# Kernel optimization log

Hardware: AMD Instinct MI355X
Metric: run time of the kernel (lower is better)

Reference implementation:

```python
import jax, jax.numpy as jnp
import numpy as np

N_BINS = 11
Q_LEN = 50
EMB = 50      # == dim_term_gating
BATCH = 256
D_LEN = 2000
EPS = 1e-8


def setup_inputs() -> dict:
    key = jax.random.key(0)
    ks = jax.random.split(key, 6)
    q_embeddings = jax.random.normal(ks[0], (BATCH, Q_LEN, EMB), jnp.float32)
    d_embeddings = jax.random.normal(ks[1], (BATCH, D_LEN, EMB), jnp.float32)
    q_embeddings_ids = jax.random.randint(ks[2], (BATCH, Q_LEN), 0, 30000)
    d_embeddings_ids = jax.random.randint(ks[3], (BATCH, D_LEN), 0, 30000)
    # linear1: Linear(n_bins*q_len, 1); gating: Linear(emb*q_len, 1, bias=False)
    W1 = jax.random.normal(ks[4], (N_BINS * Q_LEN,), jnp.float32) * 0.02
    b1 = jnp.zeros((1,), jnp.float32)
    Wg = jax.random.normal(ks[5], (EMB * Q_LEN,), jnp.float32) * 0.02
    return {
        "q_embeddings": q_embeddings,
        "d_embeddings": d_embeddings,
        "W1": W1,
        "b1": b1,
        "Wg": Wg,
        "q_embeddings_ids": q_embeddings_ids,
        "d_embeddings_ids": d_embeddings_ids,
    }


def reference(q_embeddings, d_embeddings, W1, b1, Wg, q_embeddings_ids, d_embeddings_ids):
    B, Q, E = q_embeddings.shape
    D = d_embeddings.shape[1]

    # ---- DrmmSimmat: cosine similarity between every query/doc term ----
    qn = q_embeddings / (jnp.linalg.norm(q_embeddings, axis=-1, keepdims=True) + EPS)
    dn = d_embeddings / (jnp.linalg.norm(d_embeddings, axis=-1, keepdims=True) + EPS)
    sim = jnp.einsum("bqe,bde->bqd", qn, dn)  # [B, Q, D]

    # ---- DrmmHistogram: per-query-term log-count histogram over [-1,1] ----
    # valid positions: token id != 0 (padding) in both query and doc dims
    valid = ((q_embeddings_ids > 0)[:, :, None] & (d_embeddings_ids > 0)[:, None, :])
    valid = valid.astype(jnp.float32)  # [B, Q, D]
    bins = jnp.clip(((sim + 1.000001) * 0.5 * (N_BINS - 1)).astype(jnp.int32), 0, N_BINS - 1)
    row = jnp.arange(B * Q, dtype=jnp.int32).reshape(B, Q, 1)  # histogram row per (b, q)
    flat_idx = (row * N_BINS + bins).reshape(-1)
    hist = jnp.zeros((B * Q * N_BINS,), jnp.float32).at[flat_idx].add(valid.reshape(-1))
    hist = jnp.log(hist + 1e-5).reshape(B, Q * N_BINS)

    # ---- feed-forward + term gating ----
    out_ffn = hist @ W1 + b1[0]                      # [B]
    gate = q_embeddings.reshape(B, Q * E) @ Wg       # [B]
    out_tgn = jax.nn.softmax(gate)                   # softmax over batch (faithful to F.softmax on squeezed [B])
    # torch broadcast (B,1)*(B,) -> (B,B); sum over dim=1
    matching_score = jnp.sum(out_ffn[:, None] * out_tgn[None, :], axis=1)  # [B]
    return matching_score
```

## Files before the change

### kernel.cpp

```cpp
#include <hip/hip_runtime.h>
#include <math.h>

#define BATCH 256
#define QL 50
#define EMB 50
#define DL 2000
#define NB 11
#define SEG 16
#define RPB 125
#define TPB 256
#define NKP 25
#define HB (QL * NB)

#define FOR_M5(M) M(0) M(1) M(2) M(3) M(4)
#define FOR_MN(M) \
  M(0,0) M(0,1) M(0,2) M(0,3) M(0,4) \
  M(1,0) M(1,1) M(1,2) M(1,3) M(1,4) \
  M(2,0) M(2,1) M(2,2) M(2,3) M(2,4) \
  M(3,0) M(3,1) M(3,2) M(3,3) M(3,4) \
  M(4,0) M(4,1) M(4,2) M(4,3) M(4,4)

#define DECL_ACC(m,n) float a_##m##_##n = 0.f;
#define LOAD_Q(m) const float2 qv##m = s_q2[kq + qg5 + m];
#define LOAD_D(n) const float2 dv##n = s_d2[kd + rg5 + n];
#define FMA2(m,n) a_##m##_##n = fmaf(qv##m.x, dv##n.x, a_##m##_##n); \
                  a_##m##_##n = fmaf(qv##m.y, dv##n.y, a_##m##_##n);
#define HIST_MN(m,n) if (qv_##m && dv_##n) { \
    const float s_  = a_##m##_##n * qrn##m * drn##n; \
    const float tt_ = ((s_ + 1.000001f) * 0.5f) * 10.0f; \
    int bb_ = (int)tt_; bb_ = bb_ < 0 ? 0 : (bb_ > 10 ? 10 : bb_); \
    atomicAdd(&s_hist[(qg5 + m) * NB + bb_], 1u); }

__global__ __launch_bounds__(TPB)
void sim_hist_kernel(const float* __restrict__ de,
                     const int*   __restrict__ did,
                     const float* __restrict__ qe,
                     const int*   __restrict__ qid,
                     const float* __restrict__ Wg,
                     unsigned char* __restrict__ g_hist,
                     float* __restrict__ gate,
                     int* __restrict__ cnt)
{
    const int bid = blockIdx.x;
    const int b   = bid >> 4;
    const int seg = bid & 15;
    const int t   = threadIdx.x;

    __shared__ float2   s_d2[NKP * RPB];
    __shared__ float2   s_q2[NKP * QL];
    __shared__ float    s_qrn[QL];
    __shared__ float    s_drn[RPB];
    __shared__ int      s_qv[QL];
    __shared__ int      s_dval[RPB];
    __shared__ unsigned s_hist[HB];
    __shared__ float    r2s[4];

    if (bid == 0 && t == 0) *cnt = 0;
    for (int i = t; i < HB; i += TPB) s_hist[i] = 0u;

    const float* dbase = de + ((size_t)b * DL + seg * RPB) * EMB;
    for (int i = t; i < NKP * RPB; i += TPB) {
        const int r  = i / NKP;
        const int ep = i - r * NKP;
        s_d2[ep * RPB + r] = *(const float2*)(dbase + r * EMB + 2 * ep);
    }
    const float* qbase = qe + (size_t)b * QL * EMB;
    for (int i = t; i < NKP * QL; i += TPB) {
        const int q  = i / NKP;
        const int ep = i - q * NKP;
        s_q2[ep * QL + q] = *(const float2*)(qbase + q * EMB + 2 * ep);
    }
    __syncthreads();

    if (t < RPB) {
        float ss = 0.f;
        #pragma unroll
        for (int ep = 0; ep < NKP; ++ep) {
            const float2 v = s_d2[ep * RPB + t];
            ss = fmaf(v.x, v.x, ss);
            ss = fmaf(v.y, v.y, ss);
        }
        s_drn[t]  = 1.0f / (sqrtf(ss) + 1e-8f);
        s_dval[t] = (did[(size_t)b * DL + seg * RPB + t] > 0) ? 1 : 0;
    }
    if (t < QL) {
        float ss = 0.f;
        #pragma unroll
        for (int ep = 0; ep < NKP; ++ep) {
            const float2 v = s_q2[ep * QL + t];
            ss = fmaf(v.x, v.x, ss);
            ss = fmaf(v.y, v.y, ss);
        }
        s_qrn[t] = 1.0f / (sqrtf(ss) + 1e-8f);
        s_qv[t]  = (qid[(size_t)b * QL + t] > 0) ? 1 : 0;
    }
    __syncthreads();

    if (t < 250) {
        const int qg5 = (t % 10) * 5;
        const int rg5 = (t / 10) * 5;
        FOR_MN(DECL_ACC)
        #pragma unroll 1
        for (int kp = 0; kp < NKP; ++kp) {
            const int kq = kp * QL;
            const int kd = kp * RPB;
            FOR_M5(LOAD_Q)
            FOR_M5(LOAD_D)
            FOR_MN(FMA2)
        }
        const float qrn0 = s_qrn[qg5+0], qrn1 = s_qrn[qg5+1], qrn2 = s_qrn[qg5+2],
                    qrn3 = s_qrn[qg5+3], qrn4 = s_qrn[qg5+4];
        const float drn0 = s_drn[rg5+0], drn1 = s_drn[rg5+1], drn2 = s_drn[rg5+2],
                    drn3 = s_drn[rg5+3], drn4 = s_drn[rg5+4];
        const int qv_0 = s_qv[qg5+0], qv_1 = s_qv[qg5+1], qv_2 = s_qv[qg5+2],
                  qv_3 = s_qv[qg5+3], qv_4 = s_qv[qg5+4];
        const int dv_0 = s_dval[rg5+0], dv_1 = s_dval[rg5+1], dv_2 = s_dval[rg5+2],
                  dv_3 = s_dval[rg5+3], dv_4 = s_dval[rg5+4];
        FOR_MN(HIST_MN)
    }
    __syncthreads();

    unsigned char* hout = g_hist + ((size_t)b * SEG + seg) * HB;
    for (int i = t; i < HB; i += TPB) hout[i] = (unsigned char)s_hist[i];

    if (seg == 0) {
        float a2 = 0.f;
        for (int i = t; i < QL * EMB; i += TPB)
            a2 = fmaf(qbase[i], Wg[i], a2);
        #pragma unroll
        for (int off = 32; off > 0; off >>= 1) a2 += __shfl_down(a2, off, 64);
        if ((t & 63) == 0) r2s[t >> 6] = a2;
        __syncthreads();
        if (t == 0) gate[b] = r2s[0] + r2s[1] + r2s[2] + r2s[3];
    }
}

__global__ __launch_bounds__(TPB)
void ffn_score_kernel(const unsigned char* __restrict__ g_hist,
                      const float* __restrict__ W1,
                      const float* __restrict__ bias,
                      const float* __restrict__ gate,
                      float* __restrict__ ffn,
                      int* __restrict__ cnt,
                      float* __restrict__ out)
{
    const int b = blockIdx.x;
    const int t = threadIdx.x;
    const unsigned char* hb = g_hist + (size_t)b * SEG * HB;

    float a1 = 0.f;
    for (int i = t; i < HB; i += TPB) {
        unsigned c = 0;
        #pragma unroll
        for (int s = 0; s < SEG; ++s) c += hb[s * HB + i];
        a1 = fmaf(logf((float)c + 1e-5f), W1[i], a1);
    }
    #pragma unroll
    for (int off = 32; off > 0; off >>= 1) a1 += __shfl_down(a1, off, 64);
    __shared__ float r1s[4];
    __shared__ int   s_last;
    if ((t & 63) == 0) r1s[t >> 6] = a1;
    __syncthreads();
    if (t == 0) {
        const float v = r1s[0] + r1s[1] + r1s[2] + r1s[3] + bias[0];
        atomicExch(&ffn[b], v);
        __threadfence();
        const int old = atomicAdd(cnt, 1);
        s_last = (old == BATCH - 1) ? 1 : 0;
    }
    __syncthreads();
    if (!s_last) return;
    __threadfence();

    __shared__ float buf[4];
    __shared__ float sM, sZ, sS;
    const float g = gate[t];
    const float f = atomicAdd(&ffn[t], 0.0f);

    float m = g;
    #pragma unroll
    for (int off = 32; off > 0; off >>= 1) m = fmaxf(m, __shfl_down(m, off, 64));
    if ((t & 63) == 0) buf[t >> 6] = m;
    __syncthreads();
    if (t == 0) sM = fmaxf(fmaxf(buf[0], buf[1]), fmaxf(buf[2], buf[3]));
    __syncthreads();

    const float e = expf(g - sM);
    float z = e;
    #pragma unroll
    for (int off = 32; off > 0; off >>= 1) z += __shfl_down(z, off, 64);
    __syncthreads();
    if ((t & 63) == 0) buf[t >> 6] = z;
    __syncthreads();
    if (t == 0) sZ = buf[0] + buf[1] + buf[2] + buf[3];
    __syncthreads();

    const float p = e / sZ;
    float s = p;
    #pragma unroll
    for (int off = 32; off > 0; off >>= 1) s += __shfl_down(s, off, 64);
    __syncthreads();
    if ((t & 63) == 0) buf[t >> 6] = s;
    __syncthreads();
    if (t == 0) sS = buf[0] + buf[1] + buf[2] + buf[3];
    __syncthreads();

    out[t] = f * sS;
}

extern "C" void kernel_launch(void* const* d_in, const int* in_sizes, int n_in,
                              void* d_out, int out_size, void* d_ws, size_t ws_size,
                              hipStream_t stream)
{
    const float* qe  = (const float*)d_in[0];
    const float* de  = (const float*)d_in[1];
    const float* W1  = (const float*)d_in[2];
    const float* b1  = (const float*)d_in[3];
    const float* Wg  = (const float*)d_in[4];
    const int*   qid = (const int*)d_in[5];
    const int*   did = (const int*)d_in[6];
    float* out = (float*)d_out;

    char* ws = (char*)d_ws;
    unsigned char* g_hist = (unsigned char*)ws;
    float* gate = (float*)(ws + 2252800);
    float* ffn  = gate + BATCH;
    int*   cnt  = (int*)(ffn + BATCH);

    sim_hist_kernel<<<BATCH * SEG, TPB, 0, stream>>>(de, did, qe, qid, Wg,
                                                     g_hist, gate, cnt);
    ffn_score_kernel<<<BATCH, TPB, 0, stream>>>(g_hist, W1, b1, gate, ffn, cnt, out);
}
```

Before: 234.3 us.

## Store tiles row-major with padded stride, use float4 LDS reads, fuse norm into load

Shared-memory tiles for doc and query embeddings move from a k-major float2 layout to a row-major layout with a padded stride of 52. This allows float4 LDS reads in the 5x5 register-tiled dot product, so the inner loop runs 12 iterations plus a tail instead of 25. The global-to-shared copy is now done per row by the same threads that compute the inverse norms, which removes one barrier but makes the global reads uncoalesced (one thread per row). Launch bounds now request 4 blocks per CU and the validity flags shrink to bytes.

Result: faster. 194.0 us (-17.2%).

```diff
diff --git a/kernel.cpp b/kernel.cpp
--- a/kernel.cpp
+++ b/kernel.cpp
@@ -9,7 +9,7 @@
 #define SEG 16
 #define RPB 125
 #define TPB 256
-#define NKP 25
+#define RSTRIDE 52
 #define HB (QL * NB)
 
 #define FOR_M5(M) M(0) M(1) M(2) M(3) M(4)
@@ -21,17 +21,25 @@
   M(4,0) M(4,1) M(4,2) M(4,3) M(4,4)
 
 #define DECL_ACC(m,n) float a_##m##_##n = 0.f;
-#define LOAD_Q(m) const float2 qv##m = s_q2[kq + qg5 + m];
-#define LOAD_D(n) const float2 dv##n = s_d2[kd + rg5 + n];
-#define FMA2(m,n) a_##m##_##n = fmaf(qv##m.x, dv##n.x, a_##m##_##n); \
-                  a_##m##_##n = fmaf(qv##m.y, dv##n.y, a_##m##_##n);
+#define LOAD_Q4(m) const float4 qv##m = *(const float4*)(qb0 + (m) * RSTRIDE + 4 * k);
+#define LOAD_D4(n) const float4 dv##n = *(const float4*)(db0 + (n) * RSTRIDE + 4 * k);
+#define LOAD_Q2(m) const float2 qt##m = *(const float2*)(qb0 + (m) * RSTRIDE + 48);
+#define LOAD_D2(n) const float2 dt##n = *(const float2*)(db0 + (n) * RSTRIDE + 48);
+#define FMA4(m,n) \
+  a_##m##_##n = fmaf(qv##m.x, dv##n.x, a_##m##_##n); \
+  a_##m##_##n = fmaf(qv##m.y, dv##n.y, a_##m##_##n); \
+  a_##m##_##n = fmaf(qv##m.z, dv##n.z, a_##m##_##n); \
+  a_##m##_##n = fmaf(qv##m.w, dv##n.w, a_##m##_##n);
+#define FMA2T(m,n) \
+  a_##m##_##n = fmaf(qt##m.x, dt##n.x, a_##m##_##n); \
+  a_##m##_##n = fmaf(qt##m.y, dt##n.y, a_##m##_##n);
 #define HIST_MN(m,n) if (qv_##m && dv_##n) { \
     const float s_  = a_##m##_##n * qrn##m * drn##n; \
     const float tt_ = ((s_ + 1.000001f) * 0.5f) * 10.0f; \
     int bb_ = (int)tt_; bb_ = bb_ < 0 ? 0 : (bb_ > 10 ? 10 : bb_); \
     atomicAdd(&s_hist[(qg5 + m) * NB + bb_], 1u); }
 
-__global__ __launch_bounds__(TPB)
+__global__ __launch_bounds__(TPB, 4)
 void sim_hist_kernel(const float* __restrict__ de,
                      const int*   __restrict__ did,
                      const float* __restrict__ qe,
@@ -46,67 +54,64 @@
     const int seg = bid & 15;
     const int t   = threadIdx.x;
 
-    __shared__ float2   s_d2[NKP * RPB];
-    __shared__ float2   s_q2[NKP * QL];
-    __shared__ float    s_qrn[QL];
-    __shared__ float    s_drn[RPB];
-    __shared__ int      s_qv[QL];
-    __shared__ int      s_dval[RPB];
-    __shared__ unsigned s_hist[HB];
-    __shared__ float    r2s[4];
+    __shared__ __align__(16) float s_d[RPB * RSTRIDE];
+    __shared__ __align__(16) float s_q[QL * RSTRIDE];
+    __shared__ float         s_drn[RPB];
+    __shared__ float         s_qrn[QL];
+    __shared__ unsigned char s_dval[RPB];
+    __shared__ unsigned char s_qv[QL];
+    __shared__ unsigned      s_hist[HB];
+    __shared__ float         r2s[4];
 
     if (bid == 0 && t == 0) *cnt = 0;
     for (int i = t; i < HB; i += TPB) s_hist[i] = 0u;
 
-    const float* dbase = de + ((size_t)b * DL + seg * RPB) * EMB;
-    for (int i = t; i < NKP * RPB; i += TPB) {
-        const int r  = i / NKP;
-        const int ep = i - r * NKP;
-        s_d2[ep * RPB + r] = *(const float2*)(dbase + r * EMB + 2 * ep);
-    }
-    const float* qbase = qe + (size_t)b * QL * EMB;
-    for (int i = t; i < NKP * QL; i += TPB) {
-        const int q  = i / NKP;
-        const int ep = i - q * NKP;
-        s_q2[ep * QL + q] = *(const float2*)(qbase + q * EMB + 2 * ep);
-    }
-    __syncthreads();
-
     if (t < RPB) {
+        const float* src = de + ((size_t)b * DL + seg * RPB + t) * EMB;
+        float* dst = s_d + t * RSTRIDE;
         float ss = 0.f;
         #pragma unroll
-        for (int ep = 0; ep < NKP; ++ep) {
-            const float2 v = s_d2[ep * RPB + t];
+        for (int ep = 0; ep < 25; ++ep) {
+            const float2 v = *(const float2*)(src + 2 * ep);
             ss = fmaf(v.x, v.x, ss);
             ss = fmaf(v.y, v.y, ss);
+            *(float2*)(dst + 2 * ep) = v;
         }
         s_drn[t]  = 1.0f / (sqrtf(ss) + 1e-8f);
         s_dval[t] = (did[(size_t)b * DL + seg * RPB + t] > 0) ? 1 : 0;
-    }
-    if (t < QL) {
+    } else if (t >= 128 && t < 128 + QL) {
+        const int j = t - 128;
+        const float* src = qe + ((size_t)b * QL + j) * EMB;
+        float* dst = s_q + j * RSTRIDE;
         float ss = 0.f;
         #pragma unroll
-        for (int ep = 0; ep < NKP; ++ep) {
-            const float2 v = s_q2[ep * QL + t];
+        for (int ep = 0; ep < 25; ++ep) {
+            const float2 v = *(const float2*)(src + 2 * ep);
             ss = fmaf(v.x, v.x, ss);
             ss = fmaf(v.y, v.y, ss);
-        }
-        s_qrn[t] = 1.0f / (sqrtf(ss) + 1e-8f);
-        s_qv[t]  = (qid[(size_t)b * QL + t] > 0) ? 1 : 0;
+            *(float2*)(dst + 2 * ep) = v;
+        }
+        s_qrn[j] = 1.0f / (sqrtf(ss) + 1e-8f);
+        s_qv[j]  = (qid[(size_t)b * QL + j] > 0) ? 1 : 0;
     }
     __syncthreads();
 
     if (t < 250) {
         const int qg5 = (t % 10) * 5;
         const int rg5 = (t / 10) * 5;
+        const float* qb0 = s_q + qg5 * RSTRIDE;
+        const float* db0 = s_d + rg5 * RSTRIDE;
         FOR_MN(DECL_ACC)
         #pragma unroll 1
-        for (int kp = 0; kp < NKP; ++kp) {
-            const int kq = kp * QL;
-            const int kd = kp * RPB;
-            FOR_M5(LOAD_Q)
-            FOR_M5(LOAD_D)
-            FOR_MN(FMA2)
+        for (int k = 0; k < 12; ++k) {
+            FOR_M5(LOAD_Q4)
+            FOR_M5(LOAD_D4)
+            FOR_MN(FMA4)
+        }
+        {
+            FOR_M5(LOAD_Q2)
+            FOR_M5(LOAD_D2)
+            FOR_MN(FMA2T)
         }
         const float qrn0 = s_qrn[qg5+0], qrn1 = s_qrn[qg5+1], qrn2 = s_qrn[qg5+2],
                     qrn3 = s_qrn[qg5+3], qrn4 = s_qrn[qg5+4];
@@ -124,6 +129,7 @@
     for (int i = t; i < HB; i += TPB) hout[i] = (unsigned char)s_hist[i];
 
     if (seg == 0) {
+        const float* qbase = qe + (size_t)b * QL * EMB;
         float a2 = 0.f;
         for (int i = t; i < QL * EMB; i += TPB)
             a2 = fmaf(qbase[i], Wg[i], a2);
```
